# Kernel optimization log

Measured on AMD Instinct MI355X. Metric: run time of the kernel, lower is better.

## Reference

```python
import jax, jax.numpy as jnp
import numpy as np

MARGIN = 0.5


def _pairwise_dist(x):
    # Euclidean cdist via ||a||^2 + ||b||^2 - 2ab, with safe sqrt.
    sq = jnp.sum(x * x, axis=-1)  # (N,)
    d2 = sq[:, None] + sq[None, :] - 2.0 * (x @ x.T)
    d2 = jnp.maximum(d2, 0.0)
    return jnp.sqrt(jnp.where(d2 > 0.0, d2, 1.0)) * (d2 > 0.0)


def setup_inputs() -> dict:
    key = jax.random.key(0)
    k1, k2 = jax.random.split(key)
    N, D = 8192, 128
    embeddings = jax.random.normal(k1, (N, D), dtype=jnp.float32)
    labels = jax.random.randint(k2, (N,), 0, 7, dtype=jnp.int64)
    return {"embeddings": embeddings, "labels": labels}


def reference(embeddings, labels):
    N = embeddings.shape[0]
    dist = _pairwise_dist(embeddings)  # (N, N)
    same = labels[:, None] == labels[None, :]
    eye = jnp.eye(N, dtype=bool)
    pos_mask = same & ~eye
    neg_mask = ~same
    big = jnp.asarray(jnp.finfo(dist.dtype).max, dist.dtype)
    # hardest positive: max dist among same-label (excl. self)
    pos_dist = jnp.max(jnp.where(pos_mask, dist, -big), axis=1)
    # hardest negative: min dist among different-label
    neg_dist = jnp.min(jnp.where(neg_mask, dist, big), axis=1)
    valid = jnp.any(pos_mask, axis=1) & jnp.any(neg_mask, axis=1)
    per_row = jax.nn.relu(pos_dist - neg_dist + MARGIN)
    loss_sum = jnp.sum(jnp.where(valid, per_row, 0.0))
    count = jnp.sum(valid)
    return loss_sum / jnp.maximum(count, 1).astype(loss_sum.dtype)
```

## Files before the change

### kernel.cpp

```cpp
#include <hip/hip_runtime.h>

#define N 8192
#define D 128
#define MARGIN 0.5f
#define FLT_BIG 3.402823466e+38f

typedef __bf16 bf16x8 __attribute__((ext_vector_type(8)));
typedef float f32x4 __attribute__((ext_vector_type(4)));
typedef unsigned short u16x8 __attribute__((ext_vector_type(8)));

__device__ __forceinline__ unsigned short f2bf_rne(float f) {
  unsigned u = __float_as_uint(f);
  u += 0x7FFFu + ((u >> 16) & 1u);
  return (unsigned short)(u >> 16);
}

#define FRAG_OFF(tile, k, lane) ((size_t)(tile) * 2048 + (size_t)(k) * 512 + (size_t)(lane) * 8)

__global__ void k_prep(const float* __restrict__ x, const int* __restrict__ lab,
                       unsigned short* __restrict__ xb, float* __restrict__ sq,
                       unsigned* __restrict__ posw, unsigned* __restrict__ negw,
                       unsigned* __restrict__ hist, float* __restrict__ acc,
                       unsigned* __restrict__ ticket) {
  const int t = threadIdx.x;
  const int row = blockIdx.x * 16 + (t >> 4);
  const int c = t & 15;
  const float4 v0 = ((const float4*)x)[row * 32 + c * 2];
  const float4 v1 = ((const float4*)x)[row * 32 + c * 2 + 1];
  u16x8 o;
  o[0] = f2bf_rne(v0.x); o[1] = f2bf_rne(v0.y);
  o[2] = f2bf_rne(v0.z); o[3] = f2bf_rne(v0.w);
  o[4] = f2bf_rne(v1.x); o[5] = f2bf_rne(v1.y);
  o[6] = f2bf_rne(v1.z); o[7] = f2bf_rne(v1.w);
  *(u16x8*)(xb + FRAG_OFF(row >> 4, c >> 2, ((c & 3) * 16) + (row & 15))) = o;
  float s = v0.x * v0.x + v0.y * v0.y + v0.z * v0.z + v0.w * v0.w +
            v1.x * v1.x + v1.y * v1.y + v1.z * v1.z + v1.w * v1.w;
#pragma unroll
  for (int off = 1; off < 16; off <<= 1) s += __shfl_xor(s, off, 64);
  if (c == 0) {
    sq[row] = s;
    posw[row] = 0u;
    negw[row] = 0x7F800000u;
  }

  if (blockIdx.x == 0) {
    __shared__ unsigned h[8];
    if (t < 8) h[t] = 0u;
    __syncthreads();
    unsigned long long cA = 0ull, cB = 0ull;
#pragma unroll
    for (int it = 0; it < 32; ++it) {
      const int l = lab[t + it * 256] & 7;
      if (l < 4) cA += 1ull << (l * 16);
      else       cB += 1ull << ((l - 4) * 16);
    }
#pragma unroll
    for (int off = 1; off < 64; off <<= 1) {
      cA += __shfl_xor(cA, off, 64);
      cB += __shfl_xor(cB, off, 64);
    }
    if ((t & 63) == 0) {
#pragma unroll
      for (int q = 0; q < 4; ++q) {
        atomicAdd(&h[q],     (unsigned)((cA >> (q * 16)) & 0xFFFFu));
        atomicAdd(&h[4 + q], (unsigned)((cB >> (q * 16)) & 0xFFFFu));
      }
    }
    __syncthreads();
    if (t < 8) hist[t] = h[t];
    if (t == 0) { acc[0] = 0.f; acc[1] = 0.f; ticket[0] = 0u; }
  }
}

__global__ __launch_bounds__(256, 4) void k_mine(
    const unsigned short* __restrict__ xb, const float* __restrict__ sq,
    const int* __restrict__ lab, unsigned* __restrict__ posw, unsigned* __restrict__ negw) {
  const int t = threadIdx.x;
  const int w = t >> 6;
  const int lane = t & 63;
  const int col = lane & 15;
  const int quad = lane >> 4;
  const int i0 = blockIdx.x * 128 + w * 32;
  const int jbase = blockIdx.y * 256;

  bf16x8 a[2][4];
#pragma unroll
  for (int is = 0; is < 2; ++is)
#pragma unroll
    for (int k = 0; k < 4; ++k)
      a[is][k] = *(const bf16x8*)(xb + FRAG_OFF((i0 >> 4) + is, k, lane));

  int labi[2][4];
#pragma unroll
  for (int is = 0; is < 2; ++is)
#pragma unroll
    for (int r = 0; r < 4; ++r) labi[is][r] = lab[i0 + is * 16 + quad * 4 + r];

  float pos[2][4], neg[2][4];
#pragma unroll
  for (int is = 0; is < 2; ++is)
#pragma unroll
    for (int r = 0; r < 4; ++r) { pos[is][r] = -FLT_BIG; neg[is][r] = FLT_BIG; }

  const int jt0 = jbase >> 4;
  const float* sqp = sq + jbase + col;
  const int* labp = lab + jbase + col;

#pragma unroll 1
  for (int js = 0; js < 16; ++js) {
    const float sqj = sqp[js * 16];
    const int labj = labp[js * 16];
    const unsigned short* g = xb + FRAG_OFF(jt0 + js, 0, lane);
    const bf16x8 b0 = *(const bf16x8*)(g);
    const bf16x8 b1 = *(const bf16x8*)(g + 512);
    const bf16x8 b2 = *(const bf16x8*)(g + 1024);
    const bf16x8 b3 = *(const bf16x8*)(g + 1536);

    f32x4 acc0 = {0.f, 0.f, 0.f, 0.f}, acc1 = {0.f, 0.f, 0.f, 0.f};
    acc0 = __builtin_amdgcn_mfma_f32_16x16x32_bf16(a[0][0], b0, acc0, 0, 0, 0);
    acc1 = __builtin_amdgcn_mfma_f32_16x16x32_bf16(a[1][0], b0, acc1, 0, 0, 0);
    acc0 = __builtin_amdgcn_mfma_f32_16x16x32_bf16(a[0][1], b1, acc0, 0, 0, 0);
    acc1 = __builtin_amdgcn_mfma_f32_16x16x32_bf16(a[1][1], b1, acc1, 0, 0, 0);
    acc0 = __builtin_amdgcn_mfma_f32_16x16x32_bf16(a[0][2], b2, acc0, 0, 0, 0);
    acc1 = __builtin_amdgcn_mfma_f32_16x16x32_bf16(a[1][2], b2, acc1, 0, 0, 0);
    acc0 = __builtin_amdgcn_mfma_f32_16x16x32_bf16(a[0][3], b3, acc0, 0, 0, 0);
    acc1 = __builtin_amdgcn_mfma_f32_16x16x32_bf16(a[1][3], b3, acc1, 0, 0, 0);

#pragma unroll
    for (int r = 0; r < 4; ++r) {
      const float m0 = fmaf(-2.f, acc0[r], sqj);
      const float m1 = fmaf(-2.f, acc1[r], sqj);
      const bool s0 = (labi[0][r] == labj);
      const bool s1 = (labi[1][r] == labj);
      pos[0][r] = fmaxf(pos[0][r], s0 ? m0 : -FLT_BIG);
      neg[0][r] = fminf(neg[0][r], s0 ? FLT_BIG : m0);
      pos[1][r] = fmaxf(pos[1][r], s1 ? m1 : -FLT_BIG);
      neg[1][r] = fminf(neg[1][r], s1 ? FLT_BIG : m1);
    }
  }

#pragma unroll
  for (int is = 0; is < 2; ++is)
#pragma unroll
    for (int r = 0; r < 4; ++r) {
      float p = pos[is][r], n = neg[is][r];
#pragma unroll
      for (int off = 1; off < 16; off <<= 1) {
        p = fmaxf(p, __shfl_xor(p, off, 64));
        n = fminf(n, __shfl_xor(n, off, 64));
      }
      if (col == 0) {
        const int i = i0 + is * 16 + quad * 4 + r;
        const float sqi = sq[i];
        atomicMax(posw + i, __float_as_uint(fmaxf(sqi + p, 0.f)));
        atomicMin(negw + i, __float_as_uint(fmaxf(sqi + n, 0.f)));
      }
    }
}

__global__ void k_tail(const unsigned* __restrict__ posw, const unsigned* __restrict__ negw,
                       const int* __restrict__ lab, const unsigned* __restrict__ hist,
                       float* __restrict__ acc, unsigned* __restrict__ ticket,
                       float* __restrict__ out) {
  __shared__ float ls[4], cs[4];
  const int t = threadIdx.x;
  const int i = blockIdx.x * 256 + t;
  const float pd2 = __uint_as_float(posw[i]);
  const float nd2 = __uint_as_float(negw[i]);
  const unsigned cnt = hist[lab[i] & 7];
  const bool valid = (cnt >= 2u) && (cnt < (unsigned)N);
  float loss = 0.f, c = 0.f;
  if (valid) {
    loss = fmaxf(sqrtf(pd2) - sqrtf(fminf(nd2, FLT_BIG)) + MARGIN, 0.f);
    c = 1.f;
  }
#pragma unroll
  for (int off = 1; off < 64; off <<= 1) {
    loss += __shfl_xor(loss, off, 64);
    c += __shfl_xor(c, off, 64);
  }
  const int wv = t >> 6;
  if ((t & 63) == 0) { ls[wv] = loss; cs[wv] = c; }
  __syncthreads();
  if (t == 0) {
    atomicAdd(acc + 0, ls[0] + ls[1] + ls[2] + ls[3]);
    atomicAdd(acc + 1, cs[0] + cs[1] + cs[2] + cs[3]);
    __threadfence();
    const unsigned tk = atomicAdd(ticket, 1u);
    if (tk == 31u) {
      const float lsum = atomicAdd(acc + 0, 0.f);
      const float csum = atomicAdd(acc + 1, 0.f);
      out[0] = lsum / fmaxf(csum, 1.f);
    }
  }
}

extern "C" void kernel_launch(void* const* d_in, const int* in_sizes, int n_in,
                              void* d_out, int out_size, void* d_ws, size_t ws_size,
                              hipStream_t stream) {
  const float* x = (const float*)d_in[0];
  const int* lab = (const int*)d_in[1];
  char* ws = (char*)d_ws;
  unsigned short* xb = (unsigned short*)ws;
  float* sq = (float*)(ws + (size_t)N * D * 2);
  unsigned* posw = (unsigned*)((char*)sq + (size_t)N * 4);
  unsigned* negw = posw + N;
  unsigned* hist = negw + N;
  unsigned* ticket = hist + 8;
  float* acc = (float*)(ticket + 1);
  float* out = (float*)d_out;

  hipLaunchKernelGGL(k_prep, dim3(512), dim3(256), 0, stream, x, lab, xb, sq,
                     posw, negw, hist, acc, ticket);
  hipLaunchKernelGGL(k_mine, dim3(64, 32), dim3(256), 0, stream, xb, sq, lab, posw, negw);
  hipLaunchKernelGGL(k_tail, dim3(32), dim3(256), 0, stream, posw, negw, lab, hist,
                     acc, ticket, out);
}
```

Baseline: 103.7 us.

## Exploit distance-matrix symmetry with triangular tiling and fuse tail into mining kernel

The mining kernel now covers only the lower-triangular set of 128x256 tiles, enumerated by a triangular index. Each off-diagonal tile also reduces column-wise hardest positive and negative through shared-memory atomics on order-preserving keys, so both rows and columns come out of one GEMM. This roughly halves the MFMA and bf16 load work. The separate tail kernel is removed; the last block to finish, found by a global ticket, computes the final loss. The cost is extra column-reduction ALU work, shared atomics and syncs per tile, plus a serial final reduction done by a single block.

```diff
diff --git a/kernel.cpp b/kernel.cpp
--- a/kernel.cpp
+++ b/kernel.cpp
@@ -4,6 +4,7 @@
 #define D 128
 #define MARGIN 0.5f
 #define FLT_BIG 3.402823466e+38f
+#define NBLK 1056
 
 typedef __bf16 bf16x8 __attribute__((ext_vector_type(8)));
 typedef float f32x4 __attribute__((ext_vector_type(4)));
@@ -15,13 +16,21 @@
   return (unsigned short)(u >> 16);
 }
 
+__device__ __forceinline__ unsigned fkey(float f) {
+  unsigned u = __float_as_uint(f);
+  return ((int)u < 0) ? ~u : (u | 0x80000000u);
+}
+__device__ __forceinline__ float fkey_inv(unsigned k) {
+  unsigned u = ((int)k < 0) ? (k & 0x7FFFFFFFu) : ~k;
+  return __uint_as_float(u);
+}
+
 #define FRAG_OFF(tile, k, lane) ((size_t)(tile) * 2048 + (size_t)(k) * 512 + (size_t)(lane) * 8)
 
 __global__ void k_prep(const float* __restrict__ x, const int* __restrict__ lab,
                        unsigned short* __restrict__ xb, float* __restrict__ sq,
                        unsigned* __restrict__ posw, unsigned* __restrict__ negw,
-                       unsigned* __restrict__ hist, float* __restrict__ acc,
-                       unsigned* __restrict__ ticket) {
+                       unsigned* __restrict__ hist, unsigned* __restrict__ ticket) {
   const int t = threadIdx.x;
   const int row = blockIdx.x * 16 + (t >> 4);
   const int c = t & 15;
@@ -68,20 +77,42 @@
     }
     __syncthreads();
     if (t < 8) hist[t] = h[t];
-    if (t == 0) { acc[0] = 0.f; acc[1] = 0.f; ticket[0] = 0u; }
+    if (t == 0) ticket[0] = 0u;
   }
 }
 
 __global__ __launch_bounds__(256, 4) void k_mine(
     const unsigned short* __restrict__ xb, const float* __restrict__ sq,
-    const int* __restrict__ lab, unsigned* __restrict__ posw, unsigned* __restrict__ negw) {
+    const int* __restrict__ lab, unsigned* __restrict__ posw, unsigned* __restrict__ negw,
+    const unsigned* __restrict__ hist, unsigned* __restrict__ ticket,
+    float* __restrict__ out) {
+  __shared__ unsigned cposk[256], cnegk[256];
+  __shared__ float ls[4], cs[4];
+  __shared__ unsigned lastf;
+
   const int t = threadIdx.x;
   const int w = t >> 6;
   const int lane = t & 63;
   const int col = lane & 15;
   const int quad = lane >> 4;
-  const int i0 = blockIdx.x * 128 + w * 32;
-  const int jbase = blockIdx.y * 256;
+
+  int bj, bi;
+  {
+    const int T = blockIdx.x;
+    int b = (int)((sqrtf((float)(4 * T + 1)) - 1.0f) * 0.5f);
+    while (b * (b + 1) > T) --b;
+    while ((b + 1) * (b + 2) <= T) ++b;
+    bj = b;
+    bi = T - b * (b + 1);
+  }
+  const bool diag = ((bi >> 1) == bj);
+  const int i0 = bi * 128 + w * 32;
+  const int jbase = bj * 256;
+
+  if (!diag) {
+    if (t < 256) { cposk[t] = 0u; cnegk[t] = 0xFFFFFFFFu; }
+    __syncthreads();
+  }
 
   bf16x8 a[2][4];
 #pragma unroll
@@ -91,10 +122,15 @@
       a[is][k] = *(const bf16x8*)(xb + FRAG_OFF((i0 >> 4) + is, k, lane));
 
   int labi[2][4];
-#pragma unroll
-  for (int is = 0; is < 2; ++is)
-#pragma unroll
-    for (int r = 0; r < 4; ++r) labi[is][r] = lab[i0 + is * 16 + quad * 4 + r];
+  float sqi[2][4];
+#pragma unroll
+  for (int is = 0; is < 2; ++is)
+#pragma unroll
+    for (int r = 0; r < 4; ++r) {
+      const int i = i0 + is * 16 + quad * 4 + r;
+      labi[is][r] = lab[i];
+      sqi[is][r] = sq[i];
+    }
 
   float pos[2][4], neg[2][4];
 #pragma unroll
@@ -126,6 +162,7 @@
     acc0 = __builtin_amdgcn_mfma_f32_16x16x32_bf16(a[0][3], b3, acc0, 0, 0, 0);
     acc1 = __builtin_amdgcn_mfma_f32_16x16x32_bf16(a[1][3], b3, acc1, 0, 0, 0);
 
+    float cp = -FLT_BIG, cn = FLT_BIG;
 #pragma unroll
     for (int r = 0; r < 4; ++r) {
       const float m0 = fmaf(-2.f, acc0[r], sqj);
@@ -136,6 +173,24 @@
       neg[0][r] = fminf(neg[0][r], s0 ? FLT_BIG : m0);
       pos[1][r] = fmaxf(pos[1][r], s1 ? m1 : -FLT_BIG);
       neg[1][r] = fminf(neg[1][r], s1 ? FLT_BIG : m1);
+      if (!diag) {
+        const float mc0 = fmaf(-2.f, acc0[r], sqi[0][r]);
+        const float mc1 = fmaf(-2.f, acc1[r], sqi[1][r]);
+        cp = fmaxf(cp, s0 ? mc0 : -FLT_BIG);
+        cn = fminf(cn, s0 ? FLT_BIG : mc0);
+        cp = fmaxf(cp, s1 ? mc1 : -FLT_BIG);
+        cn = fminf(cn, s1 ? FLT_BIG : mc1);
+      }
+    }
+    if (!diag) {
+      cp = fmaxf(cp, __shfl_xor(cp, 16, 64));
+      cp = fmaxf(cp, __shfl_xor(cp, 32, 64));
+      cn = fminf(cn, __shfl_xor(cn, 16, 64));
+      cn = fminf(cn, __shfl_xor(cn, 32, 64));
+      if (quad == 0) {
+        atomicMax(&cposk[js * 16 + col], fkey(cp));
+        atomicMin(&cnegk[js * 16 + col], fkey(cn));
+      }
     }
   }
 
@@ -151,48 +206,51 @@
       }
       if (col == 0) {
         const int i = i0 + is * 16 + quad * 4 + r;
-        const float sqi = sq[i];
-        atomicMax(posw + i, __float_as_uint(fmaxf(sqi + p, 0.f)));
-        atomicMin(negw + i, __float_as_uint(fmaxf(sqi + n, 0.f)));
-      }
-    }
-}
-
-__global__ void k_tail(const unsigned* __restrict__ posw, const unsigned* __restrict__ negw,
-                       const int* __restrict__ lab, const unsigned* __restrict__ hist,
-                       float* __restrict__ acc, unsigned* __restrict__ ticket,
-                       float* __restrict__ out) {
-  __shared__ float ls[4], cs[4];
-  const int t = threadIdx.x;
-  const int i = blockIdx.x * 256 + t;
-  const float pd2 = __uint_as_float(posw[i]);
-  const float nd2 = __uint_as_float(negw[i]);
-  const unsigned cnt = hist[lab[i] & 7];
-  const bool valid = (cnt >= 2u) && (cnt < (unsigned)N);
-  float loss = 0.f, c = 0.f;
-  if (valid) {
-    loss = fmaxf(sqrtf(pd2) - sqrtf(fminf(nd2, FLT_BIG)) + MARGIN, 0.f);
-    c = 1.f;
+        atomicMax(posw + i, __float_as_uint(fmaxf(sqi[is][r] + p, 0.f)));
+        atomicMin(negw + i, __float_as_uint(fmaxf(sqi[is][r] + n, 0.f)));
+      }
+    }
+
+  if (!diag) {
+    __syncthreads();
+    const int j = jbase + t;
+    const float cpv = fkey_inv(cposk[t]);
+    const float cnv = fkey_inv(cnegk[t]);
+    const float sqj = sq[j];
+    atomicMax(posw + j, __float_as_uint(fmaxf(sqj + cpv, 0.f)));
+    atomicMin(negw + j, __float_as_uint(fmaxf(sqj + cnv, 0.f)));
+  }
+
+  __threadfence();
+  __syncthreads();
+  if (t == 0) lastf = (atomicAdd(ticket, 1u) == (unsigned)(NBLK - 1)) ? 1u : 0u;
+  __syncthreads();
+  if (!lastf) return;
+
+  float loss = 0.f, cnt = 0.f;
+#pragma unroll 4
+  for (int it = 0; it < 32; ++it) {
+    const int i = t + it * 256;
+    const float pd2 = __uint_as_float(
+        __hip_atomic_load(posw + i, __ATOMIC_RELAXED, __HIP_MEMORY_SCOPE_AGENT));
+    const float nd2 = __uint_as_float(
+        __hip_atomic_load(negw + i, __ATOMIC_RELAXED, __HIP_MEMORY_SCOPE_AGENT));
+    const unsigned c = hist[lab[i] & 7];
+    if (c >= 2u && c < (unsigned)N) {
+      loss += fmaxf(sqrtf(pd2) - sqrtf(fminf(nd2, FLT_BIG)) + MARGIN, 0.f);
+      cnt += 1.f;
+    }
   }
 #pragma unroll
   for (int off = 1; off < 64; off <<= 1) {
     loss += __shfl_xor(loss, off, 64);
-    c += __shfl_xor(c, off, 64);
-  }
-  const int wv = t >> 6;
-  if ((t & 63) == 0) { ls[wv] = loss; cs[wv] = c; }
+    cnt += __shfl_xor(cnt, off, 64);
+  }
+  if (lane == 0) { ls[w] = loss; cs[w] = cnt; }
   __syncthreads();
-  if (t == 0) {
-    atomicAdd(acc + 0, ls[0] + ls[1] + ls[2] + ls[3]);
-    atomicAdd(acc + 1, cs[0] + cs[1] + cs[2] + cs[3]);
-    __threadfence();
-    const unsigned tk = atomicAdd(ticket, 1u);
-    if (tk == 31u) {
-      const float lsum = atomicAdd(acc + 0, 0.f);
-      const float csum = atomicAdd(acc + 1, 0.f);
-      out[0] = lsum / fmaxf(csum, 1.f);
-    }
-  }
+  if (t == 0)
+    out[0] = (ls[0] + ls[1] + ls[2] + ls[3]) /
+             fmaxf(cs[0] + cs[1] + cs[2] + cs[3], 1.f);
 }
 
 extern "C" void kernel_launch(void* const* d_in, const int* in_sizes, int n_in,
@@ -207,12 +265,10 @@
   unsigned* negw = posw + N;
   unsigned* hist = negw + N;
   unsigned* ticket = hist + 8;
-  float* acc = (float*)(ticket + 1);
   float* out = (float*)d_out;
 
   hipLaunchKernelGGL(k_prep, dim3(512), dim3(256), 0, stream, x, lab, xb, sq,
-                     posw, negw, hist, acc, ticket);
-  hipLaunchKernelGGL(k_mine, dim3(64, 32), dim3(256), 0, stream, xb, sq, lab, posw, negw);
-  hipLaunchKernelGGL(k_tail, dim3(32), dim3(256), 0, stream, posw, negw, lab, hist,
-                     acc, ticket, out);
-}
+                     posw, negw, hist, ticket);
+  hipLaunchKernelGGL(k_mine, dim3(NBLK), dim3(256), 0, stream, xb, sq, lab,
+                     posw, negw, hist, ticket, out);
+}
```

Result: slower. 175.4 us (+69.0%).

## Stage B tiles through LDS via async loads and fuse tail reduction into mining kernel

Applied to the files above, without the earlier changes.

The mining loop no longer has each of the four waves read all four B k-fragments from global memory. Each wave now loads one fragment into a double-buffered LDS tile with global_load_lds, and all waves then read the shared tile, so global traffic for B drops by four times. This adds a block barrier on every iteration. Separately, the tail kernel is removed: the last block to finish, found with a ticket counter, computes the final loss itself, saving one kernel launch in exchange for a serial 8192-row reduction inside a single block.

```diff
diff --git a/kernel.cpp b/kernel.cpp
--- a/kernel.cpp
+++ b/kernel.cpp
@@ -4,6 +4,7 @@
 #define D 128
 #define MARGIN 0.5f
 #define FLT_BIG 3.402823466e+38f
+#define NBLK 2048
 
 typedef __bf16 bf16x8 __attribute__((ext_vector_type(8)));
 typedef float f32x4 __attribute__((ext_vector_type(4)));
@@ -15,13 +16,18 @@
   return (unsigned short)(u >> 16);
 }
 
+__device__ __forceinline__ void stage16(const void* g, void* l) {
+  __builtin_amdgcn_global_load_lds(
+      (const __attribute__((address_space(1))) void*)g,
+      (__attribute__((address_space(3))) void*)l, 16, 0, 0);
+}
+
 #define FRAG_OFF(tile, k, lane) ((size_t)(tile) * 2048 + (size_t)(k) * 512 + (size_t)(lane) * 8)
 
 __global__ void k_prep(const float* __restrict__ x, const int* __restrict__ lab,
                        unsigned short* __restrict__ xb, float* __restrict__ sq,
                        unsigned* __restrict__ posw, unsigned* __restrict__ negw,
-                       unsigned* __restrict__ hist, float* __restrict__ acc,
-                       unsigned* __restrict__ ticket) {
+                       unsigned* __restrict__ hist, unsigned* __restrict__ ticket) {
   const int t = threadIdx.x;
   const int row = blockIdx.x * 16 + (t >> 4);
   const int c = t & 15;
@@ -68,13 +74,19 @@
     }
     __syncthreads();
     if (t < 8) hist[t] = h[t];
-    if (t == 0) { acc[0] = 0.f; acc[1] = 0.f; ticket[0] = 0u; }
+    if (t == 0) ticket[0] = 0u;
   }
 }
 
 __global__ __launch_bounds__(256, 4) void k_mine(
     const unsigned short* __restrict__ xb, const float* __restrict__ sq,
-    const int* __restrict__ lab, unsigned* __restrict__ posw, unsigned* __restrict__ negw) {
+    const int* __restrict__ lab, unsigned* __restrict__ posw, unsigned* __restrict__ negw,
+    const unsigned* __restrict__ hist, unsigned* __restrict__ ticket,
+    float* __restrict__ out) {
+  __shared__ unsigned short bst[2][4][64][8];
+  __shared__ float ls[4], cs[4];
+  __shared__ unsigned lastf;
+
   const int t = threadIdx.x;
   const int w = t >> 6;
   const int lane = t & 63;
@@ -82,6 +94,7 @@
   const int quad = lane >> 4;
   const int i0 = blockIdx.x * 128 + w * 32;
   const int jbase = blockIdx.y * 256;
+  const int jt0 = jbase >> 4;
 
   bf16x8 a[2][4];
 #pragma unroll
@@ -102,19 +115,25 @@
 #pragma unroll
     for (int r = 0; r < 4; ++r) { pos[is][r] = -FLT_BIG; neg[is][r] = FLT_BIG; }
 
-  const int jt0 = jbase >> 4;
   const float* sqp = sq + jbase + col;
   const int* labp = lab + jbase + col;
 
+#define STAGE(js_, b_) \
+  stage16(xb + FRAG_OFF(jt0 + (js_), w, lane), &bst[b_][w][0][0])
+
+  STAGE(0, 0);
+  __syncthreads();
+
 #pragma unroll 1
   for (int js = 0; js < 16; ++js) {
+    const int p = js & 1;
+    if (js < 15) STAGE(js + 1, p ^ 1);
     const float sqj = sqp[js * 16];
     const int labj = labp[js * 16];
-    const unsigned short* g = xb + FRAG_OFF(jt0 + js, 0, lane);
-    const bf16x8 b0 = *(const bf16x8*)(g);
-    const bf16x8 b1 = *(const bf16x8*)(g + 512);
-    const bf16x8 b2 = *(const bf16x8*)(g + 1024);
-    const bf16x8 b3 = *(const bf16x8*)(g + 1536);
+    const bf16x8 b0 = *(const bf16x8*)&bst[p][0][lane][0];
+    const bf16x8 b1 = *(const bf16x8*)&bst[p][1][lane][0];
+    const bf16x8 b2 = *(const bf16x8*)&bst[p][2][lane][0];
+    const bf16x8 b3 = *(const bf16x8*)&bst[p][3][lane][0];
 
     f32x4 acc0 = {0.f, 0.f, 0.f, 0.f}, acc1 = {0.f, 0.f, 0.f, 0.f};
     acc0 = __builtin_amdgcn_mfma_f32_16x16x32_bf16(a[0][0], b0, acc0, 0, 0, 0);
@@ -137,7 +156,9 @@
       pos[1][r] = fmaxf(pos[1][r], s1 ? m1 : -FLT_BIG);
       neg[1][r] = fminf(neg[1][r], s1 ? FLT_BIG : m1);
     }
-  }
+    __syncthreads();
+  }
+#undef STAGE
 
 #pragma unroll
   for (int is = 0; is < 2; ++is)
@@ -156,43 +177,37 @@
         atomicMin(negw + i, __float_as_uint(fmaxf(sqi + n, 0.f)));
       }
     }
-}
-
-__global__ void k_tail(const unsigned* __restrict__ posw, const unsigned* __restrict__ negw,
-                       const int* __restrict__ lab, const unsigned* __restrict__ hist,
-                       float* __restrict__ acc, unsigned* __restrict__ ticket,
-                       float* __restrict__ out) {
-  __shared__ float ls[4], cs[4];
-  const int t = threadIdx.x;
-  const int i = blockIdx.x * 256 + t;
-  const float pd2 = __uint_as_float(posw[i]);
-  const float nd2 = __uint_as_float(negw[i]);
-  const unsigned cnt = hist[lab[i] & 7];
-  const bool valid = (cnt >= 2u) && (cnt < (unsigned)N);
-  float loss = 0.f, c = 0.f;
-  if (valid) {
-    loss = fmaxf(sqrtf(pd2) - sqrtf(fminf(nd2, FLT_BIG)) + MARGIN, 0.f);
-    c = 1.f;
+
+  __syncthreads();
+  __threadfence();
+  if (t == 0) lastf = (atomicAdd(ticket, 1u) == (unsigned)(NBLK - 1)) ? 1u : 0u;
+  __syncthreads();
+  if (!lastf) return;
+
+  float loss = 0.f, cnt = 0.f;
+#pragma unroll 4
+  for (int it = 0; it < 32; ++it) {
+    const int i = t + it * 256;
+    const float pd2 = __uint_as_float(
+        __hip_atomic_load(posw + i, __ATOMIC_RELAXED, __HIP_MEMORY_SCOPE_AGENT));
+    const float nd2 = __uint_as_float(
+        __hip_atomic_load(negw + i, __ATOMIC_RELAXED, __HIP_MEMORY_SCOPE_AGENT));
+    const unsigned c = hist[lab[i] & 7];
+    if (c >= 2u && c < (unsigned)N) {
+      loss += fmaxf(sqrtf(pd2) - sqrtf(fminf(nd2, FLT_BIG)) + MARGIN, 0.f);
+      cnt += 1.f;
+    }
   }
 #pragma unroll
   for (int off = 1; off < 64; off <<= 1) {
     loss += __shfl_xor(loss, off, 64);
-    c += __shfl_xor(c, off, 64);
-  }
-  const int wv = t >> 6;
-  if ((t & 63) == 0) { ls[wv] = loss; cs[wv] = c; }
-  __syncthreads();
-  if (t == 0) {
-    atomicAdd(acc + 0, ls[0] + ls[1] + ls[2] + ls[3]);
-    atomicAdd(acc + 1, cs[0] + cs[1] + cs[2] + cs[3]);
-    __threadfence();
-    const unsigned tk = atomicAdd(ticket, 1u);
-    if (tk == 31u) {
-      const float lsum = atomicAdd(acc + 0, 0.f);
-      const float csum = atomicAdd(acc + 1, 0.f);
-      out[0] = lsum / fmaxf(csum, 1.f);
-    }
-  }
+    cnt += __shfl_xor(cnt, off, 64);
+  }
+  if (lane == 0) { ls[w] = loss; cs[w] = cnt; }
+  __syncthreads();
+  if (t == 0)
+    out[0] = (ls[0] + ls[1] + ls[2] + ls[3]) /
+             fmaxf(cs[0] + cs[1] + cs[2] + cs[3], 1.f);
 }
 
 extern "C" void kernel_launch(void* const* d_in, const int* in_sizes, int n_in,
@@ -207,12 +222,10 @@
   unsigned* negw = posw + N;
   unsigned* hist = negw + N;
   unsigned* ticket = hist + 8;
-  float* acc = (float*)(ticket + 1);
   float* out = (float*)d_out;
 
   hipLaunchKernelGGL(k_prep, dim3(512), dim3(256), 0, stream, x, lab, xb, sq,
-                     posw, negw, hist, acc, ticket);
-  hipLaunchKernelGGL(k_mine, dim3(64, 32), dim3(256), 0, stream, xb, sq, lab, posw, negw);
-  hipLaunchKernelGGL(k_tail, dim3(32), dim3(256), 0, stream, posw, negw, lab, hist,
-                     acc, ticket, out);
-}
+                     posw, negw, hist, ticket);
+  hipLaunchKernelGGL(k_mine, dim3(64, 32), dim3(256), 0, stream, xb, sq, lab,
+                     posw, negw, hist, ticket, out);
+}
```

New measurement: 241.0 us. 132% more time.
